# Kernel optimization log

Hardware: AMD Instinct MI355X
Metric: run time of the kernel (lower is better)

The kernel has to match this reference:

```python
import jax, jax.numpy as jnp
import numpy as np

EPS = 1e-10
WS = 5  # window_size
PAD = WS // 2


def _conv(x, k, pad_h, pad_w):
    # x: [N,1,H,W], k: [1,1,kh,kw], 'same'-style explicit padding
    return jax.lax.conv_general_dilated(
        x, k, window_strides=(1, 1),
        padding=[(pad_h, pad_h), (pad_w, pad_w)],
        dimension_numbers=("NCHW", "OIHW", "NCHW"))


def setup_inputs() -> dict:
    key = jax.random.key(0)
    B, C, Fr, T = 8, 2, 256, 2048
    spectrogram = jax.random.normal(key, (B, C, Fr, T), dtype=jnp.float32)
    # Gaussian kernel (window_size=5, sigma=1.0)
    c = WS // 2
    coords = jnp.arange(WS, dtype=jnp.float32) - c
    yy, xx = jnp.meshgrid(coords, coords, indexing="ij")
    g = jnp.exp(-(xx ** 2 + yy ** 2) / 2.0)
    gaussian_kernel = (g / g.sum()).reshape(1, 1, WS, WS)
    # Sobel kernels / 8
    sobel_x = (jnp.array([[-1, 0, 1], [-2, 0, 2], [-1, 0, 1]], jnp.float32) / 8.0).reshape(1, 1, 3, 3)
    sobel_y = (jnp.array([[-1, -2, -1], [0, 0, 0], [1, 2, 1]], jnp.float32) / 8.0).reshape(1, 1, 3, 3)
    # Harmonic kernel: 7x1 [-1,0,0,2,0,0,-1]
    hk = jnp.zeros(7, jnp.float32).at[0].set(-1.0).at[3].set(2.0).at[6].set(-1.0)
    harmonic_kernel = hk.reshape(1, 1, 7, 1)
    return {"spectrogram": spectrogram, "gaussian_kernel": gaussian_kernel,
            "sobel_x": sobel_x, "sobel_y": sobel_y, "harmonic_kernel": harmonic_kernel}


def _forward(spectrogram, gaussian_kernel, sobel_x, sobel_y, harmonic_kernel):
    B, C, Fr, T = spectrogram.shape
    # Per-channel 1-in/1-out convs == fold channels into batch.
    x = spectrogram.reshape(B * C, 1, Fr, T)

    grad_freq = _conv(x, sobel_y, 1, 1)
    grad_time = _conv(x, sobel_x, 1, 1)
    magnitude = jnp.sqrt(grad_freq ** 2 + grad_time ** 2 + EPS)
    angle = jnp.arctan2(grad_freq, grad_time + EPS)

    # ---- entropy (structure-tensor eigenvalue entropy) ----
    vx = magnitude * jnp.cos(angle)
    vy = magnitude * jnp.sin(angle)
    vxx = _conv(vx * vx, gaussian_kernel, PAD, PAD)
    vyy = _conv(vy * vy, gaussian_kernel, PAD, PAD)
    vxy = _conv(vx * vy, gaussian_kernel, PAD, PAD)
    trace = vxx + vyy
    det = vxx * vyy - vxy * vxy
    disc = jnp.sqrt(jnp.maximum(trace * trace - 4.0 * det, 0.0) + EPS)
    l1 = jnp.maximum((trace + disc) / 2.0, EPS)
    l2 = jnp.maximum((trace - disc) / 2.0, EPS)
    s = l1 + l2 + EPS
    p1, p2 = l1 / s, l2 / s
    entropy = -(p1 * jnp.log(p1 + EPS) + p2 * jnp.log(p2 + EPS)) / np.log(2.0)
    entropy = jnp.clip(entropy, 0.0, 1.0)

    # ---- alignment ----
    ux = jnp.cos(angle)
    uy = jnp.sin(angle)
    ux_avg = _conv(ux, gaussian_kernel, PAD, PAD)
    uy_avg = _conv(uy, gaussian_kernel, PAD, PAD)
    alignment = jnp.clip(jnp.sqrt(ux_avg ** 2 + uy_avg ** 2 + EPS), 0.0, 1.0)

    # ---- curvature ----
    dudx = _conv(ux, sobel_x, 1, 1)
    dudy = _conv(ux, sobel_y, 1, 1)
    dvdx = _conv(uy, sobel_x, 1, 1)
    dvdy = _conv(uy, sobel_y, 1, 1)
    curv = jnp.sqrt(dudx ** 2 + dudy ** 2 + dvdx ** 2 + dvdy ** 2 + EPS)
    curvature = _conv(curv, gaussian_kernel, PAD, PAD)

    # ---- harmonic coherence ----
    harm = jnp.abs(_conv(x, harmonic_kernel, 3, 0))
    local_energy = _conv(x ** 2, gaussian_kernel, PAD, PAD)
    harmonic = jnp.clip(harm / (local_energy + EPS), 0.0, 1.0)

    # ---- temporal stability: inverse temporal gradient magnitude, smoothed ----
    temporal = _conv(1.0 / (1.0 + jnp.abs(grad_time)), gaussian_kernel, PAD, PAD)
    temporal = jnp.clip(temporal, 0.0, 1.0)

    # ---- spectral flow: smoothed frequency-gradient magnitude ----
    spectral = jnp.clip(_conv(jnp.abs(grad_freq), gaussian_kernel, PAD, PAD), 0.0, 1.0)

    def chan_mean(f):  # [B*C,1,F,T] -> [B,1,F,T]
        return f.reshape(B, C, Fr, T).mean(axis=1, keepdims=True)

    return (chan_mean(entropy), chan_mean(alignment), chan_mean(curvature),
            chan_mean(harmonic), chan_mean(temporal), chan_mean(spectral))


def reference(spectrogram, gaussian_kernel, sobel_x, sobel_y, harmonic_kernel):
    return _forward(spectrogram, gaussian_kernel, sobel_x, sobel_y, harmonic_kernel)
```

## Files before the change

### kernel.cpp

```cpp
#include <hip/hip_runtime.h>
#include <hip/hip_fp16.h>


#define F_DIM 256
#define T_DIM 2048
#define B_DIM 8
#define C_DIM 2
#define TILE  32
#define NTHR  512

#define XROWS 40
#define XS    40
#define UROWS 38
#define US    40
#define FROWS 36
#define FS    36
#define FH2   18
#define FH4   9
#define EPSF  1e-10f

template<bool V> struct BoolC { static constexpr bool value = V; };

static __device__ __forceinline__ __half2 pack_h2(float a, float b) {
    auto v = __builtin_amdgcn_cvt_pkrtz(a, b);
    return *(__half2*)&v;
}
static __device__ __forceinline__ float clamp01(float x) {
    return fminf(fmaxf(x, 0.f), 1.f);
}
static __device__ __forceinline__ __half2 u2h(unsigned v) {
    return *(const __half2*)&v;
}

__global__ __launch_bounds__(512, 4)
void audio_struct_fused(const float* __restrict__ x_in,
                        const float* __restrict__ gk_in,
                        float* __restrict__ out)
{
    __shared__ __align__(16) float   s_x [XROWS*XS];
    __shared__ __align__(16) __half2 s_u [UROWS*US];
    __shared__ __align__(16) __half2 s_P0[FROWS*FS];
    __shared__ __align__(16) __half2 s_P1[FROWS*FS];
    __shared__ __align__(16) __half2 s_P2[FROWS*FS];
    __shared__ __align__(16) __half2 s_P3[FROWS*FS];
    __shared__ __align__(16) float   s_tmp[TILE*FS];

    const int tx  = threadIdx.x;
    const int ty  = threadIdx.y;
    const int tid = ty * 32 + tx;
    const int ryh = tid >> 4;
    const int mch = tid & 15;
    const int t0  = blockIdx.x * TILE;
    const int f0  = blockIdx.y * TILE;
    const int b   = blockIdx.z;

    float r0 = gk_in[10], r1 = gk_in[11], r2 = gk_in[12], r3 = gk_in[13], r4 = gk_in[14];
    float winv = __builtin_amdgcn_rcpf(r0 + r1 + r2 + r3 + r4);
    const float w[5] = {r0*winv, r1*winv, r2*winv, r3*winv, r4*winv};
    const __half2 wh2[5] = {pack_h2(w[0],w[0]), pack_h2(w[1],w[1]), pack_h2(w[2],w[2]),
                            pack_h2(w[3],w[3]), pack_h2(w[4],w[4])};
    const __half2 h2z    = pack_h2(0.f, 0.f);
    const __half2 two    = pack_h2(2.f, 2.f);
    const __half2 eighth = pack_h2(0.125f, 0.125f);

    auto vpass4 = [&](const __half2* src, __half2* dst) {
        const uint4* s = (const uint4*)src;
        uint4* d = (uint4*)dst;
        for (int idx = tid; idx < 16 * FH4; idx += NTHR) {
            int rg = idx / FH4, p = idx - rg * FH4;
            int base = 2 * rg * FH4 + p;
            uint4 vv[6];
            #pragma unroll
            for (int i = 0; i < 6; ++i) vv[i] = s[base + i * FH4];
            __half2 a0=h2z,a1=h2z,a2=h2z,a3=h2z, b0=h2z,b1=h2z,b2=h2z,b3=h2z;
            #pragma unroll
            for (int i = 0; i < 5; ++i) {
                a0 = __hfma2(wh2[i], u2h(vv[i].x),   a0);
                a1 = __hfma2(wh2[i], u2h(vv[i].y),   a1);
                a2 = __hfma2(wh2[i], u2h(vv[i].z),   a2);
                a3 = __hfma2(wh2[i], u2h(vv[i].w),   a3);
                b0 = __hfma2(wh2[i], u2h(vv[i+1].x), b0);
                b1 = __hfma2(wh2[i], u2h(vv[i+1].y), b1);
                b2 = __hfma2(wh2[i], u2h(vv[i+1].z), b2);
                b3 = __hfma2(wh2[i], u2h(vv[i+1].w), b3);
            }
            uint4 oa, ob;
            oa.x=*(unsigned*)&a0; oa.y=*(unsigned*)&a1; oa.z=*(unsigned*)&a2; oa.w=*(unsigned*)&a3;
            ob.x=*(unsigned*)&b0; ob.y=*(unsigned*)&b1; ob.z=*(unsigned*)&b2; ob.w=*(unsigned*)&b3;
            d[base] = oa;
            d[base + FH4] = ob;
        }
    };

    float acc[6][2];
    #pragma unroll
    for (int k = 0; k < 6; ++k)
        #pragma unroll
        for (int s = 0; s < 2; ++s) acc[k][s] = 0.0f;

    const bool interior = (f0 >= 4) && (f0 + TILE + 4 <= F_DIM) &&
                          (t0 >= 4) && (t0 + TILE + 4 <= T_DIM);

    auto phaseABC = [&](const float* xp, auto FASTC) {
        constexpr bool FAST = decltype(FASTC)::value;

        if (FAST) {
            for (int idx = tid; idx < XROWS * 10; idx += NTHR) {
                int r  = idx / 10, c4 = idx - r * 10;
                float4 v = *(const float4*)(xp + (size_t)(f0 + r - 4) * T_DIM
                                               + (t0 + c4 * 4 - 4));
                *(float4*)&s_x[r * XS + c4 * 4] = v;
            }
        } else {
            for (int idx = tid; idx < XROWS * 20; idx += NTHR) {
                int r  = idx / 20, c2 = idx - r * 20;
                int gf = f0 + r - 4;
                int gt = t0 + c2 * 2 - 4;
                float2 v = make_float2(0.f, 0.f);
                if ((unsigned)gf < (unsigned)F_DIM && (unsigned)gt < (unsigned)T_DIM)
                    v = *(const float2*)(xp + (size_t)gf * T_DIM + gt);
                *(float2*)&s_x[r * XS + c2 * 2] = v;
            }
        }
        __syncthreads();

        for (int q = tid; q < UROWS * 19; q += NTHR) {
            int r = q / 19, m = q - r * 19;
            const float2* x2p = (const float2*)s_x;
            int base = r * (XS/2) + m;
            float2 a0 = x2p[base],            b0 = x2p[base + 1];
            float2 a1 = x2p[base + (XS/2)],   b1 = x2p[base + (XS/2) + 1];
            float2 a2 = x2p[base + XS],       b2 = x2p[base + XS + 1];
            float c0 = a2.x - a0.x, c1 = a2.y - a0.y;
            float c2c = b2.x - b0.x, c3 = b2.y - b0.y;
            float s0 = fmaf(2.f, a1.x, a0.x + a2.x);
            float s1 = fmaf(2.f, a1.y, a0.y + a2.y);
            float s2 = fmaf(2.f, b1.x, b0.x + b2.x);
            float s3 = fmaf(2.f, b1.y, b0.y + b2.y);
            float gfvA = (fmaf(2.f, c1, c0) + c2c) * 0.125f;
            float gtvA = (s2 - s0) * 0.125f;
            float gfvB = (fmaf(2.f, c2c, c1) + c3) * 0.125f;
            float gtvB = (s3 - s1) * 0.125f;

            bool rin = (r >= 1) && (r < UROWS - 1);
            int  fiA = (r - 1) * FS + 2 * m - 1;
            int  gfr = f0 + r - 3;
            bool frOK = FAST || ((unsigned)gfr < (unsigned)F_DIM);

            #pragma unroll
            for (int jj = 0; jj < 2; ++jj) {
                float gfv = jj ? gfvB : gfvA;
                float gtv = jj ? gtvB : gtvA;
                int   ccI = 2 * m + jj;
                bool  okI = true;
                if (!FAST) {
                    int gtc = t0 + ccI - 3;
                    okI = frOK & ((unsigned)gtc < (unsigned)T_DIM);
                }
                float ux = 0.f, uy = 0.f, trp = 0.f, dfp = 0.f, sxy = 0.f,
                      tin = 0.f, sf = 0.f;
                if (okI) {
                    float gte = gtv + EPSF;
                    float g2f = gfv * gfv;
                    float d2  = fmaf(gte, gte, g2f);
                    float rh  = __builtin_amdgcn_rsqf(d2);
                    ux = gte * rh;
                    uy = gfv * rh;
                    float m2 = fmaf(gtv, gtv, g2f) + EPSF;
                    trp = m2;
                    dfp = m2 * (ux - uy) * (ux + uy);
                    sxy = m2 * ux * uy;
                    tin = __builtin_amdgcn_rcpf(1.0f + fabsf(gtv));
                    sf  = fabsf(gfv);
                }
                s_u[r * US + ccI + 1] = pack_h2(ux, uy);
                bool pv = rin && (jj ? (m <= 17) : (m >= 1));
                if (pv) {
                    int fi = fiA + jj;
                    s_P0[fi] = pack_h2(trp, dfp);
                    s_P1[fi] = pack_h2(sxy, tin);
                    s_P2[fi] = pack_h2(sf, 0.f);
                }
            }
        }
        __syncthreads();

        for (int q = tid; q < FROWS * FH4; q += NTHR) {
            int r = q / FH4, Q = q - r * FH4;
            const uint4* su4 = (const uint4*)s_u;
            int base = r * 10 + Q;
            uint4 ta4 = su4[base],      tb4 = su4[base + 1];
            uint4 ma4 = su4[base + 10], mb4 = su4[base + 11];
            uint4 ba4 = su4[base + 20], bb4 = su4[base + 21];
            __half2 t_[8] = {u2h(ta4.x),u2h(ta4.y),u2h(ta4.z),u2h(ta4.w),
                             u2h(tb4.x),u2h(tb4.y),u2h(tb4.z),u2h(tb4.w)};
            __half2 m_[8] = {u2h(ma4.x),u2h(ma4.y),u2h(ma4.z),u2h(ma4.w),
                             u2h(mb4.x),u2h(mb4.y),u2h(mb4.z),u2h(mb4.w)};
            __half2 b_[8] = {u2h(ba4.x),u2h(ba4.y),u2h(ba4.z),u2h(ba4.w),
                             u2h(bb4.x),u2h(bb4.y),u2h(bb4.z),u2h(bb4.w)};
            __half2 l_[7];
            #pragma unroll
            for (int k = 1; k <= 6; ++k) {
                __half2 s = __hadd2(t_[k], b_[k]);
                l_[k] = __hfma2(two, m_[k], s);
            }
            int gfr = f0 + r - 2;
            bool frOK = FAST || ((unsigned)gfr < (unsigned)F_DIM);
            #pragma unroll
            for (int jj = 0; jj < 4; ++jj) {
                __half2 tr = __hadd2(t_[jj+1], t_[jj+3]); tr = __hfma2(two, t_[jj+2], tr);
                __half2 br = __hadd2(b_[jj+1], b_[jj+3]); br = __hfma2(two, b_[jj+2], br);
                __half2 dx = __hmul2(__hsub2(l_[jj+3], l_[jj+1]), eighth);
                __half2 dy = __hmul2(__hsub2(br, tr), eighth);
                float2 fx = __half22float2(dx);
                float2 fy = __half22float2(dy);
                float cv = __builtin_amdgcn_sqrtf(
                    fmaf(fx.x, fx.x, fmaf(fx.y, fx.y,
                    fmaf(fy.x, fy.x, fy.y * fy.y))) + EPSF);
                int cc = 4 * Q + jj;
                if (!FAST) {
                    int gtc = t0 + cc - 2;
                    if (!(frOK & ((unsigned)gtc < (unsigned)T_DIM))) cv = 0.f;
                }
                ((__half*)s_P2)[2 * (r * FS + cc) + 1] = __float2half_rn(cv);
            }
        }
        vpass4(s_P0, (__half2*)s_tmp);
        vpass4(s_P1, s_P3);
        __syncthreads();
    };

    for (int c = 0; c < C_DIM; ++c) {
        if (c) __syncthreads();

        const float* xp = x_in + (size_t)(b * C_DIM + c) * F_DIM * T_DIM;
        if (interior) phaseABC(xp, BoolC<true>{});
        else          phaseABC(xp, BoolC<false>{});

        __half2* tmp_h2 = (__half2*)s_tmp;

        {
            const uint2* t2 = (const uint2*)tmp_h2;
            uint2 ta = t2[ryh * FH2 + mch], tb = t2[ryh * FH2 + mch + 1],
                  tc = t2[ryh * FH2 + mch + 2];
            float2 e0 = __half22float2(u2h(ta.x)), e1 = __half22float2(u2h(ta.y));
            float2 e2 = __half22float2(u2h(tb.x)), e3 = __half22float2(u2h(tb.y));
            float2 e4 = __half22float2(u2h(tc.x)), e5 = __half22float2(u2h(tc.y));
            float trc[2], dfc[2];
            trc[0] = w[0]*e0.x + w[1]*e1.x + w[2]*e2.x + w[3]*e3.x + w[4]*e4.x;
            dfc[0] = w[0]*e0.y + w[1]*e1.y + w[2]*e2.y + w[3]*e3.y + w[4]*e4.y;
            trc[1] = w[0]*e1.x + w[1]*e2.x + w[2]*e3.x + w[3]*e4.x + w[4]*e5.x;
            dfc[1] = w[0]*e1.y + w[1]*e2.y + w[2]*e3.y + w[3]*e4.y + w[4]*e5.y;

            const uint2* p3q = (const uint2*)s_P3;
            uint2 pa = p3q[ryh * FH2 + mch], pb = p3q[ryh * FH2 + mch + 1],
                  pc = p3q[ryh * FH2 + mch + 2];
            __half2 aA = h2z, aB = h2z;
            aA = __hfma2(wh2[0], u2h(pa.x), aA);
            aA = __hfma2(wh2[1], u2h(pa.y), aA);
            aA = __hfma2(wh2[2], u2h(pb.x), aA);
            aA = __hfma2(wh2[3], u2h(pb.y), aA);
            aA = __hfma2(wh2[4], u2h(pc.x), aA);
            aB = __hfma2(wh2[0], u2h(pa.y), aB);
            aB = __hfma2(wh2[1], u2h(pb.x), aB);
            aB = __hfma2(wh2[2], u2h(pb.y), aB);
            aB = __hfma2(wh2[3], u2h(pc.x), aB);
            aB = __hfma2(wh2[4], u2h(pc.y), aB);
            float2 vc[2] = {__half22float2(aA), __half22float2(aB)};
            #pragma unroll
            for (int col = 0; col < 2; ++col) {
                float trace = trc[col], diff = dfc[col];
                float2 v = vc[col];
                float disc  = __builtin_amdgcn_sqrtf(
                                  fmaxf(diff * diff + 4.f * v.x * v.x, 0.f) + EPSF);
                float l1 = fmaxf(0.5f * (trace + disc), EPSF);
                float l2 = fmaxf(0.5f * (trace - disc), EPSF);
                float inv = __builtin_amdgcn_rcpf(l1 + l2 + EPSF);
                float p1 = l1 * inv, p2 = l2 * inv;
                float ent = -(p1 * __builtin_amdgcn_logf(p1 + EPSF)
                            + p2 * __builtin_amdgcn_logf(p2 + EPSF));
                acc[0][col] += 0.5f * clamp01(ent);
                acc[4][col] += 0.5f * clamp01(v.y);
            }

            vpass4(s_P2, s_P0);
            {
                const uint2* su2 = (const uint2*)s_u;
                uint2* dP1 = (uint2*)s_P1;
                for (int idx = tid; idx < 16 * FH2; idx += NTHR) {
                    int rg = idx / FH2, p = idx - rg * FH2;
                    const uint2* sp = su2 + (2 * rg + 1) * (US/2) + 1 + p;
                    uint2 vv[6];
                    #pragma unroll
                    for (int i = 0; i < 6; ++i) vv[i] = sp[i * (US/2)];
                    __half2 a0 = h2z, a1 = h2z, b0 = h2z, b1 = h2z;
                    #pragma unroll
                    for (int i = 0; i < 5; ++i) {
                        a0 = __hfma2(wh2[i], u2h(vv[i].x),     a0);
                        a1 = __hfma2(wh2[i], u2h(vv[i].y),     a1);
                        b0 = __hfma2(wh2[i], u2h(vv[i + 1].x), b0);
                        b1 = __hfma2(wh2[i], u2h(vv[i + 1].y), b1);
                    }
                    uint2 oa; oa.x = *(const unsigned*)&a0; oa.y = *(const unsigned*)&a1;
                    uint2 ob; ob.x = *(const unsigned*)&b0; ob.y = *(const unsigned*)&b1;
                    dP1[2 * rg * FH2 + p] = oa;
                    dP1[(2 * rg + 1) * FH2 + p] = ob;
                }
            }
        }
        __syncthreads();

        {
            const uint2* p0q = (const uint2*)s_P0;
            uint2 qa = p0q[ryh * FH2 + mch], qb = p0q[ryh * FH2 + mch + 1],
                  qc = p0q[ryh * FH2 + mch + 2];
            __half2 sA = h2z, sB = h2z;
            sA = __hfma2(wh2[0], u2h(qa.x), sA);
            sA = __hfma2(wh2[1], u2h(qa.y), sA);
            sA = __hfma2(wh2[2], u2h(qb.x), sA);
            sA = __hfma2(wh2[3], u2h(qb.y), sA);
            sA = __hfma2(wh2[4], u2h(qc.x), sA);
            sB = __hfma2(wh2[0], u2h(qa.y), sB);
            sB = __hfma2(wh2[1], u2h(qb.x), sB);
            sB = __hfma2(wh2[2], u2h(qb.y), sB);
            sB = __hfma2(wh2[3], u2h(qc.x), sB);
            sB = __hfma2(wh2[4], u2h(qc.y), sB);
            float2 s0 = __half22float2(sA), s1 = __half22float2(sB);
            acc[5][0] += 0.5f * clamp01(s0.x);  acc[2][0] += 0.5f * s0.y;
            acc[5][1] += 0.5f * clamp01(s1.x);  acc[2][1] += 0.5f * s1.y;

            const uint2* p1q = (const uint2*)s_P1;
            uint2 ra = p1q[ryh * FH2 + mch], rb = p1q[ryh * FH2 + mch + 1],
                  rc = p1q[ryh * FH2 + mch + 2];
            __half2 uA = h2z, uB = h2z;
            uA = __hfma2(wh2[0], u2h(ra.x), uA);
            uA = __hfma2(wh2[1], u2h(ra.y), uA);
            uA = __hfma2(wh2[2], u2h(rb.x), uA);
            uA = __hfma2(wh2[3], u2h(rb.y), uA);
            uA = __hfma2(wh2[4], u2h(rc.x), uA);
            uB = __hfma2(wh2[0], u2h(ra.y), uB);
            uB = __hfma2(wh2[1], u2h(rb.x), uB);
            uB = __hfma2(wh2[2], u2h(rb.y), uB);
            uB = __hfma2(wh2[3], u2h(rc.x), uB);
            uB = __hfma2(wh2[4], u2h(rc.y), uB);
            float2 u0 = __half22float2(uA), u1 = __half22float2(uB);
            acc[1][0] += 0.5f * clamp01(
                __builtin_amdgcn_sqrtf(u0.x * u0.x + u0.y * u0.y + EPSF));
            acc[1][1] += 0.5f * clamp01(
                __builtin_amdgcn_sqrtf(u1.x * u1.x + u1.y * u1.y + EPSF));

            const float2* sx2 = (const float2*)s_x;
            float2* dt2 = (float2*)s_tmp;
            for (int idx = tid; idx < 16 * FH2; idx += NTHR) {
                int rg = idx / FH2, p = idx - rg * FH2;
                const float2* sp = sx2 + (2 * rg + 2) * (XS/2) + 1 + p;
                float2 sq[6];
                #pragma unroll
                for (int i = 0; i < 6; ++i) {
                    float2 v = sp[i * (XS/2)];
                    sq[i] = make_float2(v.x * v.x, v.y * v.y);
                }
                float aA = 0.f, bA = 0.f, aB = 0.f, bB = 0.f;
                #pragma unroll
                for (int i = 0; i < 5; ++i) {
                    aA = fmaf(w[i], sq[i].x,     aA);
                    bA = fmaf(w[i], sq[i].y,     bA);
                    aB = fmaf(w[i], sq[i + 1].x, aB);
                    bB = fmaf(w[i], sq[i + 1].y, bB);
                }
                dt2[2 * rg * FH2 + p] = make_float2(aA, bA);
                dt2[(2 * rg + 1) * FH2 + p] = make_float2(aB, bB);
            }
        }
        __syncthreads();

        {
            const float2* tf = (const float2*)s_tmp;
            float2 q0 = tf[ryh * FH2 + mch], q1 = tf[ryh * FH2 + mch + 1],
                   q2 = tf[ryh * FH2 + mch + 2];
            float le0 = w[0]*q0.x + w[1]*q0.y + w[2]*q1.x + w[3]*q1.y + w[4]*q2.x;
            float le1 = w[0]*q0.y + w[1]*q1.x + w[2]*q1.y + w[3]*q2.x + w[4]*q2.y;
            const float2* sxf = (const float2*)s_x;
            float2 xm  = sxf[(ryh + 1) * (XS/2) + mch + 2];
            float2 x0v = sxf[(ryh + 4) * (XS/2) + mch + 2];
            float2 xpv = sxf[(ryh + 7) * (XS/2) + mch + 2];
            float hA = fabsf(2.f * x0v.x - xm.x - xpv.x);
            float hB = fabsf(2.f * x0v.y - xm.y - xpv.y);
            acc[3][0] += 0.5f * clamp01(hA * __builtin_amdgcn_rcpf(le0 + EPSF));
            acc[3][1] += 0.5f * clamp01(hB * __builtin_amdgcn_rcpf(le1 + EPSF));
        }
    }

    const size_t plane = (size_t)B_DIM * F_DIM * T_DIM;
    const size_t base  = (size_t)b * F_DIM * T_DIM
                       + (size_t)(f0 + ryh) * T_DIM + t0 + 2 * mch;
    #pragma unroll
    for (int k = 0; k < 6; ++k)
        *(float2*)(out + k * plane + base) = make_float2(acc[k][0], acc[k][1]);
}

extern "C" void kernel_launch(void* const* d_in, const int* in_sizes, int n_in,
                              void* d_out, int out_size, void* d_ws, size_t ws_size,
                              hipStream_t stream) {
    const float* x  = (const float*)d_in[0];
    const float* gk = (const float*)d_in[1];
    float* out = (float*)d_out;
    dim3 grid(T_DIM / TILE, F_DIM / TILE, B_DIM);
    dim3 block(32, 16);
    audio_struct_fused<<<grid, block, 0, stream>>>(x, gk, out);
}
```

Before: 200.4 us.

## Interleave P0/P1 planes into one uint2 buffer and reuse shared scratch

Merges the two half2 partial-product planes (trace/diff and sxy/temporal) into a single interleaved uint2 array, so one vertical blur pass over wider uint4 rows replaces two separate passes. The horizontal pass then reads both quantities from the same uint4 loads. The Sobel stage now has each thread compute two rows, sharing loaded s_x rows, and later scratch buffers are aliased onto freed regions. Shared memory use drops, which may help occupancy, but the aliasing offsets and staging are delicate.

```diff
diff --git a/kernel.cpp b/kernel.cpp
--- a/kernel.cpp
+++ b/kernel.cpp
@@ -17,6 +17,7 @@
 #define FS    36
 #define FH2   18
 #define FH4   9
+#define PPW4  18
 #define EPSF  1e-10f
 
 template<bool V> struct BoolC { static constexpr bool value = V; };
@@ -37,13 +38,11 @@
                         const float* __restrict__ gk_in,
                         float* __restrict__ out)
 {
-    __shared__ __align__(16) float   s_x [XROWS*XS];
-    __shared__ __align__(16) __half2 s_u [UROWS*US];
-    __shared__ __align__(16) __half2 s_P0[FROWS*FS];
-    __shared__ __align__(16) __half2 s_P1[FROWS*FS];
-    __shared__ __align__(16) __half2 s_P2[FROWS*FS];
-    __shared__ __align__(16) __half2 s_P3[FROWS*FS];
-    __shared__ __align__(16) float   s_tmp[TILE*FS];
+    __shared__ __align__(16) float   s_x  [XROWS*XS];
+    __shared__ __align__(16) __half2 s_u  [UROWS*US];
+    __shared__ __align__(16) uint2   s_PP [FROWS*FS];
+    __shared__ __align__(16) uint2   s_PPv[TILE*FS];
+    __shared__ __align__(16) __half2 s_P2 [FROWS*FS];
 
     const int tx  = threadIdx.x;
     const int ty  = threadIdx.y;
@@ -63,15 +62,15 @@
     const __half2 two    = pack_h2(2.f, 2.f);
     const __half2 eighth = pack_h2(0.125f, 0.125f);
 
-    auto vpass4 = [&](const __half2* src, __half2* dst) {
-        const uint4* s = (const uint4*)src;
-        uint4* d = (uint4*)dst;
-        for (int idx = tid; idx < 16 * FH4; idx += NTHR) {
-            int rg = idx / FH4, p = idx - rg * FH4;
-            int base = 2 * rg * FH4 + p;
+    auto vpassPP = [&]() {
+        const uint4* s = (const uint4*)s_PP;
+        uint4* d = (uint4*)s_PPv;
+        for (int idx = tid; idx < 16 * PPW4; idx += NTHR) {
+            int rg = idx / PPW4, p = idx - rg * PPW4;
+            int base = 2 * rg * PPW4 + p;
             uint4 vv[6];
             #pragma unroll
-            for (int i = 0; i < 6; ++i) vv[i] = s[base + i * FH4];
+            for (int i = 0; i < 6; ++i) vv[i] = s[base + i * PPW4];
             __half2 a0=h2z,a1=h2z,a2=h2z,a3=h2z, b0=h2z,b1=h2z,b2=h2z,b3=h2z;
             #pragma unroll
             for (int i = 0; i < 5; ++i) {
@@ -88,6 +87,35 @@
             oa.x=*(unsigned*)&a0; oa.y=*(unsigned*)&a1; oa.z=*(unsigned*)&a2; oa.w=*(unsigned*)&a3;
             ob.x=*(unsigned*)&b0; ob.y=*(unsigned*)&b1; ob.z=*(unsigned*)&b2; ob.w=*(unsigned*)&b3;
             d[base] = oa;
+            d[base + PPW4] = ob;
+        }
+    };
+
+    auto vpass4 = [&](const __half2* src, __half2* dst) {
+        const uint4* s = (const uint4*)src;
+        uint4* d = (uint4*)dst;
+        for (int idx = tid; idx < 16 * FH4; idx += NTHR) {
+            int rg = idx / FH4, p = idx - rg * FH4;
+            int base = 2 * rg * FH4 + p;
+            uint4 vv[6];
+            #pragma unroll
+            for (int i = 0; i < 6; ++i) vv[i] = s[base + i * FH4];
+            __half2 a0=h2z,a1=h2z,a2=h2z,a3=h2z, b0=h2z,b1=h2z,b2=h2z,b3=h2z;
+            #pragma unroll
+            for (int i = 0; i < 5; ++i) {
+                a0 = __hfma2(wh2[i], u2h(vv[i].x),   a0);
+                a1 = __hfma2(wh2[i], u2h(vv[i].y),   a1);
+                a2 = __hfma2(wh2[i], u2h(vv[i].z),   a2);
+                a3 = __hfma2(wh2[i], u2h(vv[i].w),   a3);
+                b0 = __hfma2(wh2[i], u2h(vv[i+1].x), b0);
+                b1 = __hfma2(wh2[i], u2h(vv[i+1].y), b1);
+                b2 = __hfma2(wh2[i], u2h(vv[i+1].z), b2);
+                b3 = __hfma2(wh2[i], u2h(vv[i+1].w), b3);
+            }
+            uint4 oa, ob;
+            oa.x=*(unsigned*)&a0; oa.y=*(unsigned*)&a1; oa.z=*(unsigned*)&a2; oa.w=*(unsigned*)&a3;
+            ob.x=*(unsigned*)&b0; ob.y=*(unsigned*)&b1; ob.z=*(unsigned*)&b2; ob.w=*(unsigned*)&b3;
+            d[base] = oa;
             d[base + FH4] = ob;
         }
     };
@@ -124,62 +152,73 @@
         }
         __syncthreads();
 
-        for (int q = tid; q < UROWS * 19; q += NTHR) {
-            int r = q / 19, m = q - r * 19;
+        if (tid < 19 * 19) {
+            int g = tid / 19, m = tid - g * 19;
             const float2* x2p = (const float2*)s_x;
-            int base = r * (XS/2) + m;
-            float2 a0 = x2p[base],            b0 = x2p[base + 1];
-            float2 a1 = x2p[base + (XS/2)],   b1 = x2p[base + (XS/2) + 1];
-            float2 a2 = x2p[base + XS],       b2 = x2p[base + XS + 1];
-            float c0 = a2.x - a0.x, c1 = a2.y - a0.y;
-            float c2c = b2.x - b0.x, c3 = b2.y - b0.y;
-            float s0 = fmaf(2.f, a1.x, a0.x + a2.x);
-            float s1 = fmaf(2.f, a1.y, a0.y + a2.y);
-            float s2 = fmaf(2.f, b1.x, b0.x + b2.x);
-            float s3 = fmaf(2.f, b1.y, b0.y + b2.y);
-            float gfvA = (fmaf(2.f, c1, c0) + c2c) * 0.125f;
-            float gtvA = (s2 - s0) * 0.125f;
-            float gfvB = (fmaf(2.f, c2c, c1) + c3) * 0.125f;
-            float gtvB = (s3 - s1) * 0.125f;
-
-            bool rin = (r >= 1) && (r < UROWS - 1);
-            int  fiA = (r - 1) * FS + 2 * m - 1;
-            int  gfr = f0 + r - 3;
-            bool frOK = FAST || ((unsigned)gfr < (unsigned)F_DIM);
-
-            #pragma unroll
-            for (int jj = 0; jj < 2; ++jj) {
-                float gfv = jj ? gfvB : gfvA;
-                float gtv = jj ? gtvB : gtvA;
-                int   ccI = 2 * m + jj;
-                bool  okI = true;
-                if (!FAST) {
-                    int gtc = t0 + ccI - 3;
-                    okI = frOK & ((unsigned)gtc < (unsigned)T_DIM);
-                }
-                float ux = 0.f, uy = 0.f, trp = 0.f, dfp = 0.f, sxy = 0.f,
-                      tin = 0.f, sf = 0.f;
-                if (okI) {
-                    float gte = gtv + EPSF;
-                    float g2f = gfv * gfv;
-                    float d2  = fmaf(gte, gte, g2f);
-                    float rh  = __builtin_amdgcn_rsqf(d2);
-                    ux = gte * rh;
-                    uy = gfv * rh;
-                    float m2 = fmaf(gtv, gtv, g2f) + EPSF;
-                    trp = m2;
-                    dfp = m2 * (ux - uy) * (ux + uy);
-                    sxy = m2 * ux * uy;
-                    tin = __builtin_amdgcn_rcpf(1.0f + fabsf(gtv));
-                    sf  = fabsf(gfv);
-                }
-                s_u[r * US + ccI + 1] = pack_h2(ux, uy);
-                bool pv = rin && (jj ? (m <= 17) : (m >= 1));
-                if (pv) {
-                    int fi = fiA + jj;
-                    s_P0[fi] = pack_h2(trp, dfp);
-                    s_P1[fi] = pack_h2(sxy, tin);
-                    s_P2[fi] = pack_h2(sf, 0.f);
+            int base = (2 * g) * (XS/2) + m;
+            float2 A0 = x2p[base],      B0 = x2p[base + 1];
+            float2 A1 = x2p[base + 20], B1 = x2p[base + 21];
+            float2 A2 = x2p[base + 40], B2 = x2p[base + 41];
+            float2 A3 = x2p[base + 60], B3 = x2p[base + 61];
+            #pragma unroll
+            for (int rr = 0; rr < 2; ++rr) {
+                float2 a0 = rr ? A1 : A0, b0 = rr ? B1 : B0;
+                float2 a1 = rr ? A2 : A1, b1 = rr ? B2 : B1;
+                float2 a2 = rr ? A3 : A2, b2 = rr ? B3 : B2;
+                int r = 2 * g + rr;
+                float c0 = a2.x - a0.x, c1 = a2.y - a0.y;
+                float c2c = b2.x - b0.x, c3 = b2.y - b0.y;
+                float s0 = fmaf(2.f, a1.x, a0.x + a2.x);
+                float s1 = fmaf(2.f, a1.y, a0.y + a2.y);
+                float s2 = fmaf(2.f, b1.x, b0.x + b2.x);
+                float s3 = fmaf(2.f, b1.y, b0.y + b2.y);
+                float gfvA = (fmaf(2.f, c1, c0) + c2c) * 0.125f;
+                float gtvA = (s2 - s0) * 0.125f;
+                float gfvB = (fmaf(2.f, c2c, c1) + c3) * 0.125f;
+                float gtvB = (s3 - s1) * 0.125f;
+
+                bool rin = (r >= 1) && (r < UROWS - 1);
+                int  fiA = (r - 1) * FS + 2 * m - 1;
+                int  gfr = f0 + r - 3;
+                bool frOK = FAST || ((unsigned)gfr < (unsigned)F_DIM);
+
+                #pragma unroll
+                for (int jj = 0; jj < 2; ++jj) {
+                    float gfv = jj ? gfvB : gfvA;
+                    float gtv = jj ? gtvB : gtvA;
+                    int   ccI = 2 * m + jj;
+                    bool  okI = true;
+                    if (!FAST) {
+                        int gtc = t0 + ccI - 3;
+                        okI = frOK & ((unsigned)gtc < (unsigned)T_DIM);
+                    }
+                    float ux = 0.f, uy = 0.f, trp = 0.f, dfp = 0.f, sxy = 0.f,
+                          tin = 0.f, sf = 0.f;
+                    if (okI) {
+                        float gte = gtv + EPSF;
+                        float g2f = gfv * gfv;
+                        float d2  = fmaf(gte, gte, g2f);
+                        float rh  = __builtin_amdgcn_rsqf(d2);
+                        ux = gte * rh;
+                        uy = gfv * rh;
+                        float m2 = fmaf(gtv, gtv, g2f) + EPSF;
+                        trp = m2;
+                        dfp = m2 * (ux - uy) * (ux + uy);
+                        sxy = m2 * ux * uy;
+                        tin = __builtin_amdgcn_rcpf(1.0f + fabsf(gtv));
+                        sf  = fabsf(gfv);
+                    }
+                    s_u[r * US + ccI + 1] = pack_h2(ux, uy);
+                    bool pv = rin && (jj ? (m <= 17) : (m >= 1));
+                    if (pv) {
+                        int fi = fiA + jj;
+                        __half2 h0 = pack_h2(trp, dfp);
+                        __half2 h1 = pack_h2(sxy, tin);
+                        uint2 pp;
+                        pp.x = *(unsigned*)&h0; pp.y = *(unsigned*)&h1;
+                        s_PP[fi] = pp;
+                        s_P2[fi] = pack_h2(sf, 0.f);
+                    }
                 }
             }
         }
@@ -225,8 +264,7 @@
                 ((__half*)s_P2)[2 * (r * FS + cc) + 1] = __float2half_rn(cv);
             }
         }
-        vpass4(s_P0, (__half2*)s_tmp);
-        vpass4(s_P1, s_P3);
+        vpassPP();
         __syncthreads();
     };
 
@@ -237,35 +275,35 @@
         if (interior) phaseABC(xp, BoolC<true>{});
         else          phaseABC(xp, BoolC<false>{});
 
-        __half2* tmp_h2 = (__half2*)s_tmp;
+        __half2* scrA  = (__half2*)s_PP;
+        uint2*   scrB  = (uint2*)((char*)s_PP + 5184);
 
         {
-            const uint2* t2 = (const uint2*)tmp_h2;
-            uint2 ta = t2[ryh * FH2 + mch], tb = t2[ryh * FH2 + mch + 1],
-                  tc = t2[ryh * FH2 + mch + 2];
-            float2 e0 = __half22float2(u2h(ta.x)), e1 = __half22float2(u2h(ta.y));
-            float2 e2 = __half22float2(u2h(tb.x)), e3 = __half22float2(u2h(tb.y));
-            float2 e4 = __half22float2(u2h(tc.x)), e5 = __half22float2(u2h(tc.y));
+            const uint4* v4 = (const uint4*)s_PPv;
+            uint4 qa = v4[ryh * PPW4 + mch], qb = v4[ryh * PPW4 + mch + 1],
+                  qc = v4[ryh * PPW4 + mch + 2];
+            float2 e0 = __half22float2(u2h(qa.x)), e1 = __half22float2(u2h(qa.z));
+            float2 e2 = __half22float2(u2h(qb.x)), e3 = __half22float2(u2h(qb.z));
+            float2 e4 = __half22float2(u2h(qc.x)), e5 = __half22float2(u2h(qc.z));
             float trc[2], dfc[2];
             trc[0] = w[0]*e0.x + w[1]*e1.x + w[2]*e2.x + w[3]*e3.x + w[4]*e4.x;
             dfc[0] = w[0]*e0.y + w[1]*e1.y + w[2]*e2.y + w[3]*e3.y + w[4]*e4.y;
             trc[1] = w[0]*e1.x + w[1]*e2.x + w[2]*e3.x + w[3]*e4.x + w[4]*e5.x;
             dfc[1] = w[0]*e1.y + w[1]*e2.y + w[2]*e3.y + w[3]*e4.y + w[4]*e5.y;
 
-            const uint2* p3q = (const uint2*)s_P3;
-            uint2 pa = p3q[ryh * FH2 + mch], pb = p3q[ryh * FH2 + mch + 1],
-                  pc = p3q[ryh * FH2 + mch + 2];
+            __half2 st0 = u2h(qa.y), st1 = u2h(qa.w), st2 = u2h(qb.y),
+                    st3 = u2h(qb.w), st4 = u2h(qc.y), st5 = u2h(qc.w);
             __half2 aA = h2z, aB = h2z;
-            aA = __hfma2(wh2[0], u2h(pa.x), aA);
-            aA = __hfma2(wh2[1], u2h(pa.y), aA);
-            aA = __hfma2(wh2[2], u2h(pb.x), aA);
-            aA = __hfma2(wh2[3], u2h(pb.y), aA);
-            aA = __hfma2(wh2[4], u2h(pc.x), aA);
-            aB = __hfma2(wh2[0], u2h(pa.y), aB);
-            aB = __hfma2(wh2[1], u2h(pb.x), aB);
-            aB = __hfma2(wh2[2], u2h(pb.y), aB);
-            aB = __hfma2(wh2[3], u2h(pc.x), aB);
-            aB = __hfma2(wh2[4], u2h(pc.y), aB);
+            aA = __hfma2(wh2[0], st0, aA);
+            aA = __hfma2(wh2[1], st1, aA);
+            aA = __hfma2(wh2[2], st2, aA);
+            aA = __hfma2(wh2[3], st3, aA);
+            aA = __hfma2(wh2[4], st4, aA);
+            aB = __hfma2(wh2[0], st1, aB);
+            aB = __hfma2(wh2[1], st2, aB);
+            aB = __hfma2(wh2[2], st3, aB);
+            aB = __hfma2(wh2[3], st4, aB);
+            aB = __hfma2(wh2[4], st5, aB);
             float2 vc[2] = {__half22float2(aA), __half22float2(aB)};
             #pragma unroll
             for (int col = 0; col < 2; ++col) {
@@ -283,10 +321,9 @@
                 acc[4][col] += 0.5f * clamp01(v.y);
             }
 
-            vpass4(s_P2, s_P0);
+            vpass4(s_P2, scrA);
             {
                 const uint2* su2 = (const uint2*)s_u;
-                uint2* dP1 = (uint2*)s_P1;
                 for (int idx = tid; idx < 16 * FH2; idx += NTHR) {
                     int rg = idx / FH2, p = idx - rg * FH2;
                     const uint2* sp = su2 + (2 * rg + 1) * (US/2) + 1 + p;
@@ -303,15 +340,15 @@
                     }
                     uint2 oa; oa.x = *(const unsigned*)&a0; oa.y = *(const unsigned*)&a1;
                     uint2 ob; ob.x = *(const unsigned*)&b0; ob.y = *(const unsigned*)&b1;
-                    dP1[2 * rg * FH2 + p] = oa;
-                    dP1[(2 * rg + 1) * FH2 + p] = ob;
+                    scrB[2 * rg * FH2 + p] = oa;
+                    scrB[(2 * rg + 1) * FH2 + p] = ob;
                 }
             }
         }
         __syncthreads();
 
         {
-            const uint2* p0q = (const uint2*)s_P0;
+            const uint2* p0q = (const uint2*)scrA;
             uint2 qa = p0q[ryh * FH2 + mch], qb = p0q[ryh * FH2 + mch + 1],
                   qc = p0q[ryh * FH2 + mch + 2];
             __half2 sA = h2z, sB = h2z;
@@ -329,7 +366,7 @@
             acc[5][0] += 0.5f * clamp01(s0.x);  acc[2][0] += 0.5f * s0.y;
             acc[5][1] += 0.5f * clamp01(s1.x);  acc[2][1] += 0.5f * s1.y;
 
-            const uint2* p1q = (const uint2*)s_P1;
+            const uint2* p1q = (const uint2*)scrB;
             uint2 ra = p1q[ryh * FH2 + mch], rb = p1q[ryh * FH2 + mch + 1],
                   rc = p1q[ryh * FH2 + mch + 2];
             __half2 uA = h2z, uB = h2z;
@@ -350,7 +387,7 @@
                 __builtin_amdgcn_sqrtf(u1.x * u1.x + u1.y * u1.y + EPSF));
 
             const float2* sx2 = (const float2*)s_x;
-            float2* dt2 = (float2*)s_tmp;
+            float2* dt2 = (float2*)s_P2;
             for (int idx = tid; idx < 16 * FH2; idx += NTHR) {
                 int rg = idx / FH2, p = idx - rg * FH2;
                 const float2* sp = sx2 + (2 * rg + 2) * (XS/2) + 1 + p;
@@ -375,7 +412,7 @@
         __syncthreads();
 
         {
-            const float2* tf = (const float2*)s_tmp;
+            const float2* tf = (const float2*)s_P2;
             float2 q0 = tf[ryh * FH2 + mch], q1 = tf[ryh * FH2 + mch + 1],
                    q2 = tf[ryh * FH2 + mch + 2];
             float le0 = w[0]*q0.x + w[1]*q0.y + w[2]*q1.x + w[3]*q1.y + w[4]*q2.x;
```

After: 204.6 us. 2.1% more time.
